# Kernel optimization log

Hardware: AMD Instinct MI355X
Metric: run time of the kernel (lower is better)

The kernel has to match this reference:

```python
import jax, jax.numpy as jnp
import numpy as np

D_MODEL = 1024
N_HEADS = 16
D_K = D_MODEL // N_HEADS
D_FF = 4096
B = 2
T = 2048


def _layernorm(x, gamma, beta, eps=1e-5):
    mu = jnp.mean(x, axis=-1, keepdims=True)
    var = jnp.var(x, axis=-1, keepdims=True)
    return (x - mu) * jax.lax.rsqrt(var + eps) * gamma + beta


def _attention(q_in, kv_in, Wq, bq, Wk, bk, Wv, bv, mask):
    # q_in: [B,Tq,D], kv_in: [B,Tk,D]; Wq/Wk/Wv: [H,D,d_k]; b*: [H,d_k]
    Q = jnp.einsum('btd,hdk->bhtk', q_in, Wq) + bq[None, :, None, :]
    K = jnp.einsum('bsd,hdk->bhsk', kv_in, Wk) + bk[None, :, None, :]
    V = jnp.einsum('bsd,hdk->bhsk', kv_in, Wv) + bv[None, :, None, :]
    scores = jnp.einsum('bhtk,bhsk->bhts', Q, K) / jnp.sqrt(jnp.asarray(D_K, Q.dtype))
    if mask is not None:
        scores = jnp.where(mask, scores, jnp.finfo(scores.dtype).min)
    attn = jax.nn.softmax(scores, axis=-1)
    out = jnp.einsum('bhts,bhsk->bhtk', attn, V)  # [B,H,Tq,d_k]
    # concat heads: [B,Tq,H*d_k] == [B,Tq,D]
    return out.transpose(0, 2, 1, 3).reshape(q_in.shape[0], q_in.shape[1], -1)


def setup_inputs() -> dict:
    key = jax.random.key(0)
    ks = jax.random.split(key, 24)
    s = 0.02
    inp = {
        'dec_input': jax.random.normal(ks[0], (B, T, D_MODEL), jnp.float32),
        'enc_output': jax.random.normal(ks[1], (B, T, D_MODEL), jnp.float32),
        # self-attention per-head weights stacked over heads
        'Wq_s': jax.random.normal(ks[2], (N_HEADS, D_MODEL, D_K), jnp.float32) * s,
        'bq_s': jnp.zeros((N_HEADS, D_K), jnp.float32),
        'Wk_s': jax.random.normal(ks[3], (N_HEADS, D_MODEL, D_K), jnp.float32) * s,
        'bk_s': jnp.zeros((N_HEADS, D_K), jnp.float32),
        'Wv_s': jax.random.normal(ks[4], (N_HEADS, D_MODEL, D_K), jnp.float32) * s,
        'bv_s': jnp.zeros((N_HEADS, D_K), jnp.float32),
        'Wo_s': jax.random.normal(ks[5], (D_MODEL, D_MODEL), jnp.float32) * s,
        'bo_s': jnp.zeros((D_MODEL,), jnp.float32),
        # cross-attention per-head weights
        'Wq_c': jax.random.normal(ks[6], (N_HEADS, D_MODEL, D_K), jnp.float32) * s,
        'bq_c': jnp.zeros((N_HEADS, D_K), jnp.float32),
        'Wk_c': jax.random.normal(ks[7], (N_HEADS, D_MODEL, D_K), jnp.float32) * s,
        'bk_c': jnp.zeros((N_HEADS, D_K), jnp.float32),
        'Wv_c': jax.random.normal(ks[8], (N_HEADS, D_MODEL, D_K), jnp.float32) * s,
        'bv_c': jnp.zeros((N_HEADS, D_K), jnp.float32),
        'Wo_c': jax.random.normal(ks[9], (D_MODEL, D_MODEL), jnp.float32) * s,
        'bo_c': jnp.zeros((D_MODEL,), jnp.float32),
        # FFN
        'W1': jax.random.normal(ks[10], (D_MODEL, D_FF), jnp.float32) * s,
        'b1': jnp.zeros((D_FF,), jnp.float32),
        'W2': jax.random.normal(ks[11], (D_FF, D_MODEL), jnp.float32) * s,
        'b2': jnp.zeros((D_MODEL,), jnp.float32),
        # layernorms
        'g1': jnp.ones((D_MODEL,), jnp.float32), 'be1': jnp.zeros((D_MODEL,), jnp.float32),
        'g2': jnp.ones((D_MODEL,), jnp.float32), 'be2': jnp.zeros((D_MODEL,), jnp.float32),
        'g3': jnp.ones((D_MODEL,), jnp.float32), 'be3': jnp.zeros((D_MODEL,), jnp.float32),
    }
    return inp


def reference(dec_input, enc_output,
              Wq_s, bq_s, Wk_s, bk_s, Wv_s, bv_s, Wo_s, bo_s,
              Wq_c, bq_c, Wk_c, bk_c, Wv_c, bv_c, Wo_c, bo_c,
              W1, b1, W2, b2, g1, be1, g2, be2, g3, be3):
    Tq = dec_input.shape[1]
    causal = jnp.tril(jnp.ones((Tq, Tq), bool))[None, None, :, :]  # [1,1,T,T]
    # masked multi-head self-attention (dropout is identity in eval)
    sa = _attention(dec_input, dec_input, Wq_s, bq_s, Wk_s, bk_s, Wv_s, bv_s, causal)
    sa = sa @ Wo_s.T if False else jnp.einsum('btd,ed->bte', sa, Wo_s.T) if False else sa @ Wo_s + bo_s
    x1 = _layernorm(dec_input + sa, g1, be1)
    # cross-attention (no mask)
    ca = _attention(x1, enc_output, Wq_c, bq_c, Wk_c, bk_c, Wv_c, bv_c, None)
    ca = ca @ Wo_c + bo_c
    x2 = _layernorm(x1 + ca, g2, be2)
    # FFN
    ffn = jax.nn.relu(x2 @ W1 + b1) @ W2 + b2
    x3 = _layernorm(x2 + ffn, g3, be3)
    return x3
```

## Files before the change

kernel.cpp:

```cpp
#include <hip/hip_runtime.h>
#include <hip/hip_bf16.h>

typedef __attribute__((ext_vector_type(8))) short short8;
typedef __attribute__((ext_vector_type(4))) short short4v;
typedef __attribute__((ext_vector_type(4))) float floatx4;

#define TDIM 2048
#define BDIM 2
#define MROWS (BDIM * TDIM)

#define ASM_VMCNT0() __asm__ volatile("s_waitcnt vmcnt(0)" ::: "memory")
#define ASM_LGKM0()  __asm__ volatile("s_waitcnt lgkmcnt(0)" ::: "memory")
#define ASM_BARRIER() __asm__ volatile("s_barrier" ::: "memory")

__device__ __forceinline__ floatx4 mfma16(short4v a, short4v b, floatx4 c) {
#if defined(__HIP_DEVICE_COMPILE__)
#if __has_builtin(__builtin_amdgcn_mfma_f32_16x16x16bf16_1k)
    return __builtin_amdgcn_mfma_f32_16x16x16bf16_1k(a, b, c, 0, 0, 0);
#else
    short8 az = {a[0], a[1], a[2], a[3], 0, 0, 0, 0};
    short8 bz = {b[0], b[1], b[2], b[3], 0, 0, 0, 0};
    return __builtin_amdgcn_mfma_f32_16x16x32_bf16(az, bz, c, 0, 0, 0);
#endif
#else
    (void)a; (void)b;
    return c;
#endif
}

__device__ __forceinline__ void gload_lds16(const void* g, void* l) {
    __builtin_amdgcn_global_load_lds((const __attribute__((address_space(1))) void*)g,
                                     (__attribute__((address_space(3))) void*)l, 16, 0, 0);
}

__device__ __forceinline__ short bf16s(float x) {
    __hip_bfloat16 h = __float2bfloat16(x);
    return *(short*)&h;
}

__global__ __launch_bounds__(256) void cast2_k(const float* __restrict__ a,
                                               const float* __restrict__ b,
                                               __hip_bfloat16* __restrict__ oa,
                                               __hip_bfloat16* __restrict__ ob) {
    const int blk = blockIdx.x;
    const float* in = (blk < 4096) ? a : b;
    __hip_bfloat16* out = (blk < 4096) ? oa : ob;
    const size_t base = (size_t)(blk & 4095) * 1024 + threadIdx.x * 4;
    float4 v = *(const float4*)&in[base];
    out[base + 0] = __float2bfloat16(v.x);
    out[base + 1] = __float2bfloat16(v.y);
    out[base + 2] = __float2bfloat16(v.z);
    out[base + 3] = __float2bfloat16(v.w);
}

__device__ __forceinline__ void t32(float (*tile)[33], const float* __restrict__ in,
                                    __hip_bfloat16* __restrict__ out, int R, int C,
                                    int c0, int r0) {
    const int tx = threadIdx.x & 31, ty = threadIdx.x >> 5;
#pragma unroll
    for (int i = 0; i < 4; ++i)
        tile[ty + 8 * i][tx] = in[(size_t)(r0 + ty + 8 * i) * C + c0 + tx];
    __syncthreads();
#pragma unroll
    for (int i = 0; i < 4; ++i)
        out[(size_t)(c0 + ty + 8 * i) * R + r0 + tx] = __float2bfloat16(tile[tx][ty + 8 * i]);
}

__global__ __launch_bounds__(256) void prep_w_k(
    const float* __restrict__ Wq_s, const float* __restrict__ Wk_s, const float* __restrict__ Wv_s,
    const float* __restrict__ Wq_c, const float* __restrict__ Wk_c, const float* __restrict__ Wv_c,
    const float* __restrict__ Wo_s, const float* __restrict__ Wo_c,
    const float* __restrict__ W1, const float* __restrict__ W2,
    const float* __restrict__ bq_s, const float* __restrict__ bk_s, const float* __restrict__ bv_s,
    const float* __restrict__ bk_c, const float* __restrict__ bv_c,
    __hip_bfloat16* __restrict__ WtQKVs, __hip_bfloat16* __restrict__ WtQc,
    __hip_bfloat16* __restrict__ WtKVc, __hip_bfloat16* __restrict__ WtOs,
    __hip_bfloat16* __restrict__ WtOc, __hip_bfloat16* __restrict__ Wt1,
    __hip_bfloat16* __restrict__ Wt2,
    float* __restrict__ BiasQKVs, float* __restrict__ BiasKVc) {
    __shared__ float tile[32][33];
    const int t = blockIdx.x;
    if (t < 6144) {
        const int seg = t >> 10, tl = t & 1023;
        const float* s;
        __hip_bfloat16* d;
        if (seg == 0) { s = Wq_s; d = WtQKVs; }
        else if (seg == 1) { s = Wk_s; d = WtQKVs + 1048576; }
        else if (seg == 2) { s = Wv_s; d = WtQKVs + 2097152; }
        else if (seg == 3) { s = Wq_c; d = WtQc; }
        else if (seg == 4) { s = Wk_c; d = WtKVc; }
        else { s = Wv_c; d = WtKVc + 1048576; }
        const int slab = tl >> 6, rem = tl & 63;
        t32(tile, s + (size_t)slab * 65536, d + (size_t)slab * 65536, 1024, 64,
            (rem & 1) * 32, (rem >> 1) * 32);
    } else if (t < 8192) {
        const int rem = (t - 6144) & 1023;
        const float* s = (t < 7168) ? Wo_s : Wo_c;
        __hip_bfloat16* d = (t < 7168) ? WtOs : WtOc;
        t32(tile, s, d, 1024, 1024, (rem & 31) * 32, (rem >> 5) * 32);
    } else if (t < 12288) {
        const int rem = t - 8192;
        t32(tile, W1, Wt1, 1024, 4096, (rem & 127) * 32, (rem >> 7) * 32);
    } else if (t < 16384) {
        const int rem = t - 12288;
        t32(tile, W2, Wt2, 4096, 1024, (rem & 31) * 32, (rem >> 5) * 32);
    } else if (t < 16396) {
        const int i = (t - 16384) * 256 + threadIdx.x;
        BiasQKVs[i] = (i < 1024) ? bq_s[i] : (i < 2048 ? bk_s[i - 1024] : bv_s[i - 2048]);
    } else {
        const int i = (t - 16396) * 256 + threadIdx.x;
        BiasKVc[i] = (i < 1024) ? bk_c[i] : bv_c[i - 1024];
    }
}

__device__ __forceinline__ void gemm_core(
    const __hip_bfloat16* __restrict__ A, const __hip_bfloat16* __restrict__ Bt,
    int K, int kBeg, int kLen,
    const float* __restrict__ bias, __hip_bfloat16* __restrict__ C, int ldc,
    float* __restrict__ Pf,
    __hip_bfloat16* __restrict__ Vt, int vt_col0, int relu,
    int m0, int n0, __hip_bfloat16* sm) {
    const int tid = threadIdx.x;
    const int lane = tid & 63, wave = tid >> 6;
    const int quad = lane >> 4, l16 = lane & 15;
    const int wm = (wave >> 1) * 64, wn = (wave & 1) * 64;
    const int lrow = lane >> 3;
    const int gsw = (((lane & 7) ^ lrow)) * 8;
    const int sw7 = l16 & 7;
    const __hip_bfloat16* gA = A + (size_t)(m0 + wave * 32 + lrow) * K + kBeg + gsw;
    const __hip_bfloat16* gB = Bt + (size_t)(n0 + wave * 32 + lrow) * K + kBeg + gsw;
    __hip_bfloat16* lA = sm + wave * 2048;
    __hip_bfloat16* lB = sm + 16384 + wave * 2048;
    floatx4 acc[4][4] = {};
    const int T = kLen >> 6;
#pragma unroll
    for (int i = 0; i < 4; ++i) {
        gload_lds16(gA + (size_t)i * 8 * K, lA + i * 512);
        gload_lds16(gB + (size_t)i * 8 * K, lB + i * 512);
    }
    for (int t = 0; t < T; ++t) {
        ASM_VMCNT0();
        ASM_BARRIER();
        if (t + 1 < T) {
            const int koff = (t + 1) << 6;
            const int b = ((t + 1) & 1) * 8192;
#pragma unroll
            for (int i = 0; i < 4; ++i) {
                gload_lds16(gA + (size_t)i * 8 * K + koff, lA + b + i * 512);
                gload_lds16(gB + (size_t)i * 8 * K + koff, lB + b + i * 512);
            }
        }
        const __hip_bfloat16* cA = sm + (t & 1) * 8192;
        const __hip_bfloat16* cB = sm + 16384 + (t & 1) * 8192;
#pragma unroll
        for (int kc = 0; kc < 2; ++kc) {
            short8 af[4], bfr[4];
#pragma unroll
            for (int i = 0; i < 4; ++i) {
                af[i] = *(const short8*)&cA[(wm + i * 16 + l16) * 64 +
                                            (((kc * 4 + quad) ^ sw7) * 8)];
                bfr[i] = *(const short8*)&cB[(wn + i * 16 + l16) * 64 +
                                             (((kc * 4 + quad) ^ sw7) * 8)];
            }
#pragma unroll
            for (int mi = 0; mi < 4; ++mi)
#pragma unroll
                for (int ni = 0; ni < 4; ++ni)
                    acc[mi][ni] =
                        __builtin_amdgcn_mfma_f32_16x16x32_bf16(af[mi], bfr[ni], acc[mi][ni], 0, 0, 0);
        }
    }
    if (Pf) {
#pragma unroll
        for (int ni = 0; ni < 4; ++ni) {
            const int col = n0 + wn + ni * 16 + l16;
#pragma unroll
            for (int mi = 0; mi < 4; ++mi)
#pragma unroll
                for (int r = 0; r < 4; ++r) {
                    const int row = m0 + wm + mi * 16 + quad * 4 + r;
                    Pf[(size_t)row * ldc + col] = acc[mi][ni][r];
                }
        }
    } else {
        const bool toVt = (n0 >= vt_col0);
#pragma unroll
        for (int ni = 0; ni < 4; ++ni) {
            const int col = n0 + wn + ni * 16 + l16;
            const float bv = bias[col];
#pragma unroll
            for (int mi = 0; mi < 4; ++mi) {
                const int row0 = m0 + wm + mi * 16 + quad * 4;
                if (toVt) {
                    const int b = row0 >> 11, t0 = row0 & (TDIM - 1);
                    short4v pk;
#pragma unroll
                    for (int r = 0; r < 4; ++r) pk[r] = bf16s(acc[mi][ni][r] + bv);
                    *(short4v*)&Vt[((size_t)(b * 1024 + (col - vt_col0)) << 11) + t0] = pk;
                } else {
#pragma unroll
                    for (int r = 0; r < 4; ++r) {
                        float v = acc[mi][ni][r] + bv;
                        if (relu) v = fmaxf(v, 0.f);
                        C[(size_t)(row0 + r) * ldc + col] = __float2bfloat16(v);
                    }
                }
            }
        }
    }
}

__global__ __launch_bounds__(256) void gemm_bf16_k(const __hip_bfloat16* __restrict__ A,
                                                   const __hip_bfloat16* __restrict__ Bt,
                                                   const float* __restrict__ bias,
                                                   __hip_bfloat16* __restrict__ C,
                                                   int N, int K, int relu,
                                                   __hip_bfloat16* __restrict__ Vt, int vt_col0) {
    __shared__ __hip_bfloat16 sm[2 * 128 * 64 * 2];
    gemm_core(A, Bt, K, 0, K, bias, C, N, nullptr, Vt, vt_col0, relu,
              blockIdx.y * 128, blockIdx.x * 128, sm);
}

__global__ __launch_bounds__(256) void gemm_sk2_k(const __hip_bfloat16* __restrict__ A,
                                                  const __hip_bfloat16* __restrict__ Bt,
                                                  float* __restrict__ Pf, int N, int K) {
    __shared__ __hip_bfloat16 sm[2 * 128 * 64 * 2];
    const int z = blockIdx.z;
    gemm_core(A, Bt, K, z * (K >> 1), K >> 1, nullptr, nullptr, N,
              Pf + (size_t)z * MROWS * N, nullptr, 1 << 30, 0,
              blockIdx.y * 128, blockIdx.x * 128, sm);
}

__global__ __launch_bounds__(256) void gemm_pair_k(
    const __hip_bfloat16* __restrict__ A1, const __hip_bfloat16* __restrict__ Bt1,
    const float* __restrict__ bias1, __hip_bfloat16* __restrict__ C1, int N1, int K1,
    const __hip_bfloat16* __restrict__ A2, const __hip_bfloat16* __restrict__ Bt2,
    const float* __restrict__ bias2, __hip_bfloat16* __restrict__ C2, int N2, int K2,
    __hip_bfloat16* __restrict__ Vt2, int vtc2, int nx1) {
    __shared__ __hip_bfloat16 sm[2 * 128 * 64 * 2];
    if ((int)blockIdx.x < nx1)
        gemm_core(A1, Bt1, K1, 0, K1, bias1, C1, N1, nullptr, nullptr, 1 << 30, 0,
                  blockIdx.y * 128, blockIdx.x * 128, sm);
    else
        gemm_core(A2, Bt2, K2, 0, K2, bias2, C2, N2, nullptr, Vt2, vtc2, 0,
                  blockIdx.y * 128, (blockIdx.x - nx1) * 128, sm);
}

__device__ __forceinline__ void flash_one(
    const __hip_bfloat16* __restrict__ Q, int ldq, int qc0,
    const __hip_bfloat16* __restrict__ Kp, int ldk,
    const __hip_bfloat16* __restrict__ Vp,
    __hip_bfloat16* __restrict__ O, int causal, int q0, size_t rowb, int h,
    __hip_bfloat16* sK, __hip_bfloat16* sV) {
    const int tid = threadIdx.x, lane = tid & 63, wave = tid >> 6;
    const int quad = lane >> 4, l16 = lane & 15;
    const int lrow = lane >> 3;
    const int gsw = ((lane & 7) ^ lrow) * 8;
    const int sw7 = l16 & 7;
    short8 qf[2];
    {
        const __hip_bfloat16* qp = Q + (rowb + q0 + wave * 16 + l16) * (size_t)ldq + qc0 + h * 64;
        const float qs = 0.18033688f;
        short8 r0 = *(const short8*)(qp + quad * 8);
        short8 r1 = *(const short8*)(qp + 32 + quad * 8);
#pragma unroll
        for (int j = 0; j < 8; ++j) {
            qf[0][j] = bf16s(__uint_as_float(((unsigned)(unsigned short)r0[j]) << 16) * qs);
            qf[1][j] = bf16s(__uint_as_float(((unsigned)(unsigned short)r1[j]) << 16) * qs);
        }
    }
    short4v ones4;
#pragma unroll
    for (int j = 0; j < 4; ++j) ones4[j] = (short)0x3F80;
    floatx4 Ot[4] = {};
    floatx4 accl = {};
    const int nDiag = q0 >> 6;
    const int lastT = causal ? nDiag : (TDIM >> 6) - 1;
    ASM_LGKM0();
    ASM_BARRIER();
#pragma unroll
    for (int i = 0; i < 2; ++i) {
        const int rb = wave * 16 + i * 8;
        gload_lds16(&Kp[(rowb + rb + lrow) * (size_t)ldk + gsw], &sK[rb * 64]);
        gload_lds16(&Vp[(size_t)(rb + lrow) * TDIM + gsw], &sV[rb * 64]);
    }
    for (int t = 0; t <= lastT; ++t) {
        ASM_VMCNT0();
        ASM_BARRIER();
        if (t < lastT) {
            const int s1 = (t + 1) << 6, nb = ((t + 1) & 1) * 4096;
#pragma unroll
            for (int i = 0; i < 2; ++i) {
                const int rb = wave * 16 + i * 8;
                gload_lds16(&Kp[(rowb + s1 + rb + lrow) * (size_t)ldk + gsw], &sK[nb + rb * 64]);
                gload_lds16(&Vp[(size_t)(rb + lrow) * TDIM + s1 + gsw], &sV[nb + rb * 64]);
            }
        }
        const int cb = (t & 1) * 4096;
        floatx4 Sf[4] = {};
#pragma unroll
        for (int st = 0; st < 4; ++st) {
            short8 b0 = *(const short8*)&sK[cb + (st * 16 + l16) * 64 + ((quad ^ sw7) * 8)];
            short8 b1 = *(const short8*)&sK[cb + (st * 16 + l16) * 64 + (((4 + quad) ^ sw7) * 8)];
            Sf[st] = __builtin_amdgcn_mfma_f32_16x16x32_bf16(b0, qf[0], Sf[st], 0, 0, 0);
            Sf[st] = __builtin_amdgcn_mfma_f32_16x16x32_bf16(b1, qf[1], Sf[st], 0, 0, 0);
        }
#pragma unroll
        for (int st = 0; st < 4; ++st)
#pragma unroll
            for (int r = 0; r < 4; ++r) Sf[st][r] = exp2f(Sf[st][r]);
        if (causal && t == nDiag) {
            const int qr = wave * 16 + l16;
#pragma unroll
            for (int st = 0; st < 4; ++st)
#pragma unroll
                for (int r = 0; r < 4; ++r)
                    if (st * 16 + quad * 4 + r > qr) Sf[st][r] = 0.f;
        }
        short4v pf[4];
#pragma unroll
        for (int st = 0; st < 4; ++st)
#pragma unroll
            for (int r = 0; r < 4; ++r) pf[st][r] = bf16s(Sf[st][r]);
#pragma unroll
        for (int st = 0; st < 4; ++st) accl = mfma16(ones4, pf[st], accl);
#pragma unroll
        for (int dt = 0; dt < 4; ++dt)
#pragma unroll
            for (int st = 0; st < 4; ++st) {
                short4v av = *(const short4v*)&sV[cb + (dt * 16 + l16) * 64 +
                                                 (((st * 2 + (quad >> 1)) ^ sw7) * 8) +
                                                 (quad & 1) * 4];
                Ot[dt] = mfma16(av, pf[st], Ot[dt]);
            }
    }
    const float inv = 1.0f / accl[0];
    __hip_bfloat16* op = O + (rowb + q0 + wave * 16 + l16) * (size_t)1024 + h * 64 + quad * 4;
#pragma unroll
    for (int dt = 0; dt < 4; ++dt) {
        short4v pk;
#pragma unroll
        for (int r = 0; r < 4; ++r) pk[r] = bf16s(Ot[dt][r] * inv);
        *(short4v*)(op + dt * 16) = pk;
    }
}

__global__ __launch_bounds__(256) void flash_attn(const __hip_bfloat16* __restrict__ Q, int ldq, int qc0,
                                                  const __hip_bfloat16* __restrict__ K, int ldk, int kc0,
                                                  const __hip_bfloat16* __restrict__ Vt,
                                                  __hip_bfloat16* __restrict__ O, int causal) {
    __shared__ __hip_bfloat16 sK[2 * 64 * 64];
    __shared__ __hip_bfloat16 sV[2 * 64 * 64];
    const int bh = blockIdx.y, b = bh >> 4, h = bh & 15;
    const size_t rowb = (size_t)b * TDIM;
    const __hip_bfloat16* Kp = K + kc0 + h * 64;
    const __hip_bfloat16* Vp = Vt + ((size_t)(b * 1024 + h * 64) << 11);
    if (causal) {
        flash_one(Q, ldq, qc0, Kp, ldk, Vp, O, 1, (int)blockIdx.x * 64, rowb, h, sK, sV);
        flash_one(Q, ldq, qc0, Kp, ldk, Vp, O, 1, (31 - (int)blockIdx.x) * 64, rowb, h, sK, sV);
    } else {
        flash_one(Q, ldq, qc0, Kp, ldk, Vp, O, 0, (int)blockIdx.x * 64, rowb, h, sK, sV);
    }
}

__global__ __launch_bounds__(256) void ln2_k(const float* __restrict__ resid,
                                             const float* __restrict__ d0,
                                             const float* __restrict__ d1,
                                             const float* __restrict__ biasN,
                                             const float* __restrict__ gamma,
                                             const float* __restrict__ beta,
                                             float* __restrict__ outf,
                                             __hip_bfloat16* __restrict__ outb) {
    const int row = blockIdx.x, tid = threadIdx.x;
    const size_t base = (size_t)row * 1024;
    float x[4], s = 0.f, sq = 0.f;
#pragma unroll
    for (int i = 0; i < 4; ++i) {
        const int c = tid + 256 * i;
        x[i] = resid[base + c] + d0[base + c] + d1[base + c] + biasN[c];
        s += x[i];
        sq += x[i] * x[i];
    }
#pragma unroll
    for (int off = 32; off > 0; off >>= 1) {
        s += __shfl_down(s, off);
        sq += __shfl_down(sq, off);
    }
    __shared__ float red[8];
    if ((tid & 63) == 0) {
        red[tid >> 6] = s;
        red[4 + (tid >> 6)] = sq;
    }
    __syncthreads();
    const float S = red[0] + red[1] + red[2] + red[3];
    const float Q2 = red[4] + red[5] + red[6] + red[7];
    const float mean = S * (1.f / 1024.f);
    const float var = Q2 * (1.f / 1024.f) - mean * mean;
    const float rstd = rsqrtf(var + 1e-5f);
#pragma unroll
    for (int i = 0; i < 4; ++i) {
        const int c = tid + 256 * i;
        const float y = (x[i] - mean) * rstd * gamma[c] + beta[c];
        outf[base + c] = y;
        outb[base + c] = __float2bfloat16(y);
    }
}

extern "C" void kernel_launch(void* const* d_in, const int* in_sizes, int n_in,
                              void* d_out, int out_size, void* d_ws, size_t ws_size,
                              hipStream_t stream) {
    (void)in_sizes; (void)n_in; (void)out_size; (void)ws_size;
    const float* dec  = (const float*)d_in[0];
    const float* enc  = (const float*)d_in[1];
    const float* Wq_s = (const float*)d_in[2];
    const float* bq_s = (const float*)d_in[3];
    const float* Wk_s = (const float*)d_in[4];
    const float* bk_s = (const float*)d_in[5];
    const float* Wv_s = (const float*)d_in[6];
    const float* bv_s = (const float*)d_in[7];
    const float* Wo_s = (const float*)d_in[8];
    const float* bo_s = (const float*)d_in[9];
    const float* Wq_c = (const float*)d_in[10];
    const float* bq_c = (const float*)d_in[11];
    const float* Wk_c = (const float*)d_in[12];
    const float* bk_c = (const float*)d_in[13];
    const float* Wv_c = (const float*)d_in[14];
    const float* bv_c = (const float*)d_in[15];
    const float* Wo_c = (const float*)d_in[16];
    const float* bo_c = (const float*)d_in[17];
    const float* W1   = (const float*)d_in[18];
    const float* b1   = (const float*)d_in[19];
    const float* W2   = (const float*)d_in[20];
    const float* b2   = (const float*)d_in[21];
    const float* g1   = (const float*)d_in[22];
    const float* be1  = (const float*)d_in[23];
    const float* g2   = (const float*)d_in[24];
    const float* be2  = (const float*)d_in[25];
    const float* g3   = (const float*)d_in[26];
    const float* be3  = (const float*)d_in[27];

    char* w = (char*)d_ws;
    const size_t MB = 1ull << 20;
    __hip_bfloat16* Xdec   = (__hip_bfloat16*)(w + 0 * MB);
    __hip_bfloat16* Xenc   = (__hip_bfloat16*)(w + 8 * MB);
    __hip_bfloat16* WtQKVs = (__hip_bfloat16*)(w + 16 * MB);
    __hip_bfloat16* WtOs   = (__hip_bfloat16*)(w + 22 * MB);
    __hip_bfloat16* WtQc   = (__hip_bfloat16*)(w + 24 * MB);
    __hip_bfloat16* WtKVc  = (__hip_bfloat16*)(w + 26 * MB);
    __hip_bfloat16* WtOc   = (__hip_bfloat16*)(w + 30 * MB);
    __hip_bfloat16* Wt1    = (__hip_bfloat16*)(w + 32 * MB);
    __hip_bfloat16* Wt2    = (__hip_bfloat16*)(w + 40 * MB);
    float*          BiasQKVs = (float*)(w + 48 * MB);
    float*          BiasKVc  = (float*)(w + 48 * MB + 65536);
    __hip_bfloat16* QKV    = (__hip_bfloat16*)(w + 49 * MB);
    __hip_bfloat16* Qc     = QKV;
    __hip_bfloat16* KVc    = (__hip_bfloat16*)(w + 57 * MB);
    float*          Psplit = (float*)(w + 49 * MB);
    __hip_bfloat16* VtBuf  = (__hip_bfloat16*)(w + 73 * MB);
    __hip_bfloat16* Attn   = (__hip_bfloat16*)(w + 81 * MB);
    float*          X1f    = (float*)(w + 97 * MB);
    __hip_bfloat16* X1b    = (__hip_bfloat16*)(w + 113 * MB);
    float*          X2f    = (float*)(w + 121 * MB);
    __hip_bfloat16* X2b    = (__hip_bfloat16*)(w + 137 * MB);
    __hip_bfloat16* H1     = (__hip_bfloat16*)(w + 145 * MB);
    float*          P0     = Psplit;
    float*          P1     = Psplit + (size_t)MROWS * 1024;
    const int NOVT = 1 << 30;

    cast2_k<<<8192, 256, 0, stream>>>(dec, enc, Xdec, Xenc);
    prep_w_k<<<16404, 256, 0, stream>>>(Wq_s, Wk_s, Wv_s, Wq_c, Wk_c, Wv_c, Wo_s, Wo_c,
                                        W1, W2, bq_s, bk_s, bv_s, bk_c, bv_c,
                                        WtQKVs, WtQc, WtKVc, WtOs, WtOc, Wt1, Wt2,
                                        BiasQKVs, BiasKVc);

    gemm_bf16_k<<<dim3(24, 32), 256, 0, stream>>>(Xdec, WtQKVs, BiasQKVs, QKV, 3072, 1024, 0,
                                                  VtBuf, 2048);
    flash_attn<<<dim3(16, 32), 256, 0, stream>>>(QKV, 3072, 0, QKV, 3072, 1024, VtBuf, Attn, 1);
    gemm_sk2_k<<<dim3(8, 32, 2), 256, 0, stream>>>(Attn, WtOs, Psplit, 1024, 1024);
    ln2_k<<<MROWS, 256, 0, stream>>>(dec, P0, P1, bo_s, g1, be1, X1f, X1b);

    gemm_pair_k<<<dim3(24, 32), 256, 0, stream>>>(X1b, WtQc, bq_c, Qc, 1024, 1024,
                                                  Xenc, WtKVc, BiasKVc, KVc, 2048, 1024,
                                                  VtBuf, 1024, 8);
    flash_attn<<<dim3(32, 32), 256, 0, stream>>>(Qc, 1024, 0, KVc, 2048, 0, VtBuf, Attn, 0);
    gemm_sk2_k<<<dim3(8, 32, 2), 256, 0, stream>>>(Attn, WtOc, Psplit, 1024, 1024);
    ln2_k<<<MROWS, 256, 0, stream>>>(X1f, P0, P1, bo_c, g2, be2, X2f, X2b);

    gemm_bf16_k<<<dim3(32, 32), 256, 0, stream>>>(X2b, Wt1, b1, H1, 4096, 1024, 1,
                                                  (__hip_bfloat16*)nullptr, NOVT);
    gemm_sk2_k<<<dim3(8, 32, 2), 256, 0, stream>>>(H1, Wt2, Psplit, 1024, 4096);
    ln2_k<<<MROWS, 256, 0, stream>>>(X2f, P0, P1, b2, g3, be3, (float*)d_out, X1b);
}
```

Baseline: 546.9 us.

## Process two query tiles per flash block sharing each K/V LDS tile

Flash attention now handles two 64-row query tiles at once in a single pass over keys, so each K/V tile loaded into shared memory serves both, roughly halving K/V global traffic and barrier count. Cross-attention launches half as many blocks. The causal pairing keeps the balanced front/back split, but the shorter tile sits idle once past its diagonal. Separately, bf16 conversions are packed two at a time into vectorized stores. The cost is more registers per thread and fewer blocks, which may reduce occupancy.

```diff
diff --git a/kernel.cpp b/kernel.cpp
--- a/kernel.cpp
+++ b/kernel.cpp
@@ -38,6 +38,13 @@
     return *(short*)&h;
 }
 
+__device__ __forceinline__ short4v pk4(float a, float b, float c, float d) {
+    union { __hip_bfloat162 h2[2]; short4v s4; } u;
+    u.h2[0] = __float22bfloat162_rn(make_float2(a, b));
+    u.h2[1] = __float22bfloat162_rn(make_float2(c, d));
+    return u.s4;
+}
+
 __global__ __launch_bounds__(256) void cast2_k(const float* __restrict__ a,
                                                const float* __restrict__ b,
                                                __hip_bfloat16* __restrict__ oa,
@@ -47,10 +54,7 @@
     __hip_bfloat16* out = (blk < 4096) ? oa : ob;
     const size_t base = (size_t)(blk & 4095) * 1024 + threadIdx.x * 4;
     float4 v = *(const float4*)&in[base];
-    out[base + 0] = __float2bfloat16(v.x);
-    out[base + 1] = __float2bfloat16(v.y);
-    out[base + 2] = __float2bfloat16(v.z);
-    out[base + 3] = __float2bfloat16(v.w);
+    *(short4v*)&out[base] = pk4(v.x, v.y, v.z, v.w);
 }
 
 __device__ __forceinline__ void t32(float (*tile)[33], const float* __restrict__ in,
@@ -193,10 +197,9 @@
                 const int row0 = m0 + wm + mi * 16 + quad * 4;
                 if (toVt) {
                     const int b = row0 >> 11, t0 = row0 & (TDIM - 1);
-                    short4v pk;
-#pragma unroll
-                    for (int r = 0; r < 4; ++r) pk[r] = bf16s(acc[mi][ni][r] + bv);
-                    *(short4v*)&Vt[((size_t)(b * 1024 + (col - vt_col0)) << 11) + t0] = pk;
+                    *(short4v*)&Vt[((size_t)(b * 1024 + (col - vt_col0)) << 11) + t0] =
+                        pk4(acc[mi][ni][0] + bv, acc[mi][ni][1] + bv,
+                            acc[mi][ni][2] + bv, acc[mi][ni][3] + bv);
                 } else {
 #pragma unroll
                     for (int r = 0; r < 4; ++r) {
@@ -246,36 +249,42 @@
                   blockIdx.y * 128, (blockIdx.x - nx1) * 128, sm);
 }
 
-__device__ __forceinline__ void flash_one(
+__device__ __forceinline__ void flash_two(
     const __hip_bfloat16* __restrict__ Q, int ldq, int qc0,
     const __hip_bfloat16* __restrict__ Kp, int ldk,
     const __hip_bfloat16* __restrict__ Vp,
-    __hip_bfloat16* __restrict__ O, int causal, int q0, size_t rowb, int h,
-    __hip_bfloat16* sK, __hip_bfloat16* sV) {
+    __hip_bfloat16* __restrict__ O, int causal, int q0a, int q0b,
+    size_t rowb, int h, __hip_bfloat16* sK, __hip_bfloat16* sV) {
     const int tid = threadIdx.x, lane = tid & 63, wave = tid >> 6;
     const int quad = lane >> 4, l16 = lane & 15;
     const int lrow = lane >> 3;
     const int gsw = ((lane & 7) ^ lrow) * 8;
     const int sw7 = l16 & 7;
-    short8 qf[2];
+    const float qs = 0.18033688f;
+    short8 qfA[2], qfB[2];
     {
-        const __hip_bfloat16* qp = Q + (rowb + q0 + wave * 16 + l16) * (size_t)ldq + qc0 + h * 64;
-        const float qs = 0.18033688f;
-        short8 r0 = *(const short8*)(qp + quad * 8);
-        short8 r1 = *(const short8*)(qp + 32 + quad * 8);
-#pragma unroll
-        for (int j = 0; j < 8; ++j) {
-            qf[0][j] = bf16s(__uint_as_float(((unsigned)(unsigned short)r0[j]) << 16) * qs);
-            qf[1][j] = bf16s(__uint_as_float(((unsigned)(unsigned short)r1[j]) << 16) * qs);
+        const __hip_bfloat16* qpA = Q + (rowb + q0a + wave * 16 + l16) * (size_t)ldq + qc0 + h * 64;
+        const __hip_bfloat16* qpB = Q + (rowb + q0b + wave * 16 + l16) * (size_t)ldq + qc0 + h * 64;
+#pragma unroll
+        for (int half = 0; half < 2; ++half) {
+            short8 ra = *(const short8*)(qpA + half * 32 + quad * 8);
+            short8 rb = *(const short8*)(qpB + half * 32 + quad * 8);
+#pragma unroll
+            for (int j = 0; j < 8; ++j) {
+                qfA[half][j] = bf16s(__uint_as_float(((unsigned)(unsigned short)ra[j]) << 16) * qs);
+                qfB[half][j] = bf16s(__uint_as_float(((unsigned)(unsigned short)rb[j]) << 16) * qs);
+            }
         }
     }
     short4v ones4;
 #pragma unroll
     for (int j = 0; j < 4; ++j) ones4[j] = (short)0x3F80;
-    floatx4 Ot[4] = {};
-    floatx4 accl = {};
-    const int nDiag = q0 >> 6;
-    const int lastT = causal ? nDiag : (TDIM >> 6) - 1;
+    floatx4 OtA[4] = {}, OtB[4] = {};
+    floatx4 acclA = {}, acclB = {};
+    const int TQ = TDIM >> 6;
+    const int lastA = causal ? (q0a >> 6) : TQ - 1;
+    const int lastB = causal ? (q0b >> 6) : TQ - 1;
+    const int lastT = (lastA > lastB) ? lastA : lastB;
     ASM_LGKM0();
     ASM_BARRIER();
 #pragma unroll
@@ -297,33 +306,51 @@
             }
         }
         const int cb = (t & 1) * 4096;
-        floatx4 Sf[4] = {};
+        const bool actA = (t <= lastA), actB = (t <= lastB);
+        floatx4 SfA[4] = {}, SfB[4] = {};
 #pragma unroll
         for (int st = 0; st < 4; ++st) {
             short8 b0 = *(const short8*)&sK[cb + (st * 16 + l16) * 64 + ((quad ^ sw7) * 8)];
             short8 b1 = *(const short8*)&sK[cb + (st * 16 + l16) * 64 + (((4 + quad) ^ sw7) * 8)];
-            Sf[st] = __builtin_amdgcn_mfma_f32_16x16x32_bf16(b0, qf[0], Sf[st], 0, 0, 0);
-            Sf[st] = __builtin_amdgcn_mfma_f32_16x16x32_bf16(b1, qf[1], Sf[st], 0, 0, 0);
-        }
-#pragma unroll
-        for (int st = 0; st < 4; ++st)
-#pragma unroll
-            for (int r = 0; r < 4; ++r) Sf[st][r] = exp2f(Sf[st][r]);
-        if (causal && t == nDiag) {
-            const int qr = wave * 16 + l16;
-#pragma unroll
-            for (int st = 0; st < 4; ++st)
-#pragma unroll
-                for (int r = 0; r < 4; ++r)
-                    if (st * 16 + quad * 4 + r > qr) Sf[st][r] = 0.f;
-        }
-        short4v pf[4];
-#pragma unroll
-        for (int st = 0; st < 4; ++st)
-#pragma unroll
-            for (int r = 0; r < 4; ++r) pf[st][r] = bf16s(Sf[st][r]);
-#pragma unroll
-        for (int st = 0; st < 4; ++st) accl = mfma16(ones4, pf[st], accl);
+            if (actA) {
+                SfA[st] = __builtin_amdgcn_mfma_f32_16x16x32_bf16(b0, qfA[0], SfA[st], 0, 0, 0);
+                SfA[st] = __builtin_amdgcn_mfma_f32_16x16x32_bf16(b1, qfA[1], SfA[st], 0, 0, 0);
+            }
+            if (actB) {
+                SfB[st] = __builtin_amdgcn_mfma_f32_16x16x32_bf16(b0, qfB[0], SfB[st], 0, 0, 0);
+                SfB[st] = __builtin_amdgcn_mfma_f32_16x16x32_bf16(b1, qfB[1], SfB[st], 0, 0, 0);
+            }
+        }
+        short4v pfA[4], pfB[4];
+        const int qr = wave * 16 + l16;
+        if (actA) {
+#pragma unroll
+            for (int st = 0; st < 4; ++st) {
+#pragma unroll
+                for (int r = 0; r < 4; ++r) SfA[st][r] = exp2f(SfA[st][r]);
+                if (causal && t == lastA) {
+#pragma unroll
+                    for (int r = 0; r < 4; ++r)
+                        if (st * 16 + quad * 4 + r > qr) SfA[st][r] = 0.f;
+                }
+                pfA[st] = pk4(SfA[st][0], SfA[st][1], SfA[st][2], SfA[st][3]);
+                acclA = mfma16(ones4, pfA[st], acclA);
+            }
+        }
+        if (actB) {
+#pragma unroll
+            for (int st = 0; st < 4; ++st) {
+#pragma unroll
+                for (int r = 0; r < 4; ++r) SfB[st][r] = exp2f(SfB[st][r]);
+                if (causal && t == lastB) {
+#pragma unroll
+                    for (int r = 0; r < 4; ++r)
+                        if (st * 16 + quad * 4 + r > qr) SfB[st][r] = 0.f;
+                }
+                pfB[st] = pk4(SfB[st][0], SfB[st][1], SfB[st][2], SfB[st][3]);
+                acclB = mfma16(ones4, pfB[st], acclB);
+            }
+        }
 #pragma unroll
         for (int dt = 0; dt < 4; ++dt)
 #pragma unroll
@@ -331,17 +358,19 @@
                 short4v av = *(const short4v*)&sV[cb + (dt * 16 + l16) * 64 +
                                                  (((st * 2 + (quad >> 1)) ^ sw7) * 8) +
                                                  (quad & 1) * 4];
-                Ot[dt] = mfma16(av, pf[st], Ot[dt]);
-            }
-    }
-    const float inv = 1.0f / accl[0];
-    __hip_bfloat16* op = O + (rowb + q0 + wave * 16 + l16) * (size_t)1024 + h * 64 + quad * 4;
+                if (actA) OtA[dt] = mfma16(av, pfA[st], OtA[dt]);
+                if (actB) OtB[dt] = mfma16(av, pfB[st], OtB[dt]);
+            }
+    }
+    const float invA = 1.0f / acclA[0], invB = 1.0f / acclB[0];
+    __hip_bfloat16* opA = O + (rowb + q0a + wave * 16 + l16) * (size_t)1024 + h * 64 + quad * 4;
+    __hip_bfloat16* opB = O + (rowb + q0b + wave * 16 + l16) * (size_t)1024 + h * 64 + quad * 4;
 #pragma unroll
     for (int dt = 0; dt < 4; ++dt) {
-        short4v pk;
-#pragma unroll
-        for (int r = 0; r < 4; ++r) pk[r] = bf16s(Ot[dt][r] * inv);
-        *(short4v*)(op + dt * 16) = pk;
+        *(short4v*)(opA + dt * 16) = pk4(OtA[dt][0] * invA, OtA[dt][1] * invA,
+                                         OtA[dt][2] * invA, OtA[dt][3] * invA);
+        *(short4v*)(opB + dt * 16) = pk4(OtB[dt][0] * invB, OtB[dt][1] * invB,
+                                         OtB[dt][2] * invB, OtB[dt][3] * invB);
     }
 }
 
@@ -355,12 +384,10 @@
     const size_t rowb = (size_t)b * TDIM;
     const __hip_bfloat16* Kp = K + kc0 + h * 64;
     const __hip_bfloat16* Vp = Vt + ((size_t)(b * 1024 + h * 64) << 11);
-    if (causal) {
-        flash_one(Q, ldq, qc0, Kp, ldk, Vp, O, 1, (int)blockIdx.x * 64, rowb, h, sK, sV);
-        flash_one(Q, ldq, qc0, Kp, ldk, Vp, O, 1, (31 - (int)blockIdx.x) * 64, rowb, h, sK, sV);
-    } else {
-        flash_one(Q, ldq, qc0, Kp, ldk, Vp, O, 0, (int)blockIdx.x * 64, rowb, h, sK, sV);
-    }
+    const int bx = blockIdx.x;
+    const int q0a = bx * 64;
+    const int q0b = causal ? (31 - bx) * 64 : (bx + 16) * 64;
+    flash_two(Q, ldq, qc0, Kp, ldk, Vp, O, causal, q0a, q0b, rowb, h, sK, sV);
 }
 
 __global__ __launch_bounds__(256) void ln2_k(const float* __restrict__ resid,
@@ -482,7 +509,7 @@
     gemm_pair_k<<<dim3(24, 32), 256, 0, stream>>>(X1b, WtQc, bq_c, Qc, 1024, 1024,
                                                   Xenc, WtKVc, BiasKVc, KVc, 2048, 1024,
                                                   VtBuf, 1024, 8);
-    flash_attn<<<dim3(32, 32), 256, 0, stream>>>(Qc, 1024, 0, KVc, 2048, 0, VtBuf, Attn, 0);
+    flash_attn<<<dim3(16, 32), 256, 0, stream>>>(Qc, 1024, 0, KVc, 2048, 0, VtBuf, Attn, 0);
     gemm_sk2_k<<<dim3(8, 32, 2), 256, 0, stream>>>(Attn, WtOc, Psplit, 1024, 1024);
     ln2_k<<<MROWS, 256, 0, stream>>>(X1f, P0, P1, bo_c, g2, be2, X2f, X2b);
 
```

Result: slower. 568.0 us (+3.9%).
